# Kernel optimization log

Measured on AMD Instinct MI355X. Metric: run time of the kernel, lower is better.

## Reference

```python
import jax, jax.numpy as jnp
import numpy as np
from jax import lax

VOCAB, EMBED, HIDDEN = 32000, 512, 1024
BATCH, SEQ = 64, 512


def setup_inputs() -> dict:
    key = jax.random.key(0)
    ks = jax.random.split(key, 10)
    H, E, V = HIDDEN, EMBED, VOCAB
    s = lambda *d: 1.0 / np.sqrt(d[0])
    return {
        "x": jax.random.randint(ks[0], (BATCH, SEQ), 0, V, dtype=jnp.int32),
        "embed_table": jax.random.normal(ks[1], (V, E), jnp.float32) * 0.02,
        "Wx0": jax.random.normal(ks[2], (E, 4 * H), jnp.float32) * s(E),
        "Wh0": jax.random.normal(ks[3], (H, 4 * H), jnp.float32) * s(H),
        "b0": jnp.zeros((4 * H,), jnp.float32),
        "Wx1": jax.random.normal(ks[4], (H, 4 * H), jnp.float32) * s(H),
        "Wh1": jax.random.normal(ks[5], (H, 4 * H), jnp.float32) * s(H),
        "b1": jnp.zeros((4 * H,), jnp.float32),
        "Wout": jax.random.normal(ks[6], (H, V), jnp.float32) * s(H),
        "bout": jnp.zeros((V,), jnp.float32),
    }


def _lstm_layer(inp, Wx, Wh, b):
    # inp: [B, S, D_in] -> hidden states [B, S, H]
    B = inp.shape[0]
    H = Wh.shape[0]
    # Precompute the input projection for all timesteps (one big GEMM).
    x4 = jnp.einsum("bsd,dg->bsg", inp, Wx) + b           # [B, S, 4H]
    x4 = jnp.swapaxes(x4, 0, 1)                              # [S, B, 4H]
    h0 = jnp.zeros((B, H), inp.dtype)
    c0 = jnp.zeros((B, H), inp.dtype)

    def step(carry, xt4):
        h, c = carry
        g = xt4 + h @ Wh                                     # [B, 4H]
        i, f, gg, o = jnp.split(g, 4, axis=-1)
        c = jax.nn.sigmoid(f) * c + jax.nn.sigmoid(i) * jnp.tanh(gg)
        h = jax.nn.sigmoid(o) * jnp.tanh(c)
        return (h, c), h

    _, hs = lax.scan(step, (h0, c0), x4)                     # hs: [S, B, H]
    return jnp.swapaxes(hs, 0, 1)                            # [B, S, H]


def reference(x, embed_table, Wx0, Wh0, b0, Wx1, Wh1, b1, Wout, bout):
    emb = embed_table[x]                                      # [B, S, E]
    h1 = _lstm_layer(emb, Wx0, Wh0, b0)                       # [B, S, H]
    h2 = _lstm_layer(h1, Wx1, Wh1, b1)                        # [B, S, H]
    logits = h2[:, -1, :] @ Wout + bout                       # [B, V] (last timestep)
    return jax.nn.softmax(logits, axis=-1)
```

## Files before the change

kernel.cpp:

```cpp
#include <hip/hip_runtime.h>


#define BB 64
#define SS 512
#define EE 512
#define HH 1024
#define GG 4096
#define VV 32000

using bf16x8 = __attribute__((ext_vector_type(8))) __bf16;
using f32x4  = __attribute__((ext_vector_type(4))) float;

__device__ __forceinline__ unsigned short f2bf(float f) {
    unsigned u = __float_as_uint(f);
    unsigned r = u + 0x7FFFu + ((u >> 16) & 1u);
    return (unsigned short)(r >> 16);
}
__device__ __forceinline__ float bf2f(unsigned short u) {
    return __uint_as_float(((unsigned)u) << 16);
}
__device__ __forceinline__ float sigm(float x) {
    return 1.0f / (1.0f + expf(-x));
}
__device__ __forceinline__ bf16x8 ld_frag_coh(const unsigned long long* p) {
    union { unsigned long long u[2]; bf16x8 v; } x;
    x.u[0] = __hip_atomic_load(p,     __ATOMIC_RELAXED, __HIP_MEMORY_SCOPE_AGENT);
    x.u[1] = __hip_atomic_load(p + 1, __ATOMIC_RELAXED, __HIP_MEMORY_SCOPE_AGENT);
    return x.v;
}
__device__ __forceinline__ void gate_poll(const unsigned int* p, unsigned tgt) {
    while (__hip_atomic_load(p, __ATOMIC_RELAXED, __HIP_MEMORY_SCOPE_AGENT) < tgt)
        __builtin_amdgcn_s_sleep(1);
    __builtin_amdgcn_sched_barrier(0);
}

__global__ void pack_b(const float* __restrict__ B, unsigned short* __restrict__ out,
                       int KT, int N) {
    int bid = blockIdx.x;
    int lane = threadIdx.x;
    int nt = bid / KT, kt = bid % KT;
    int k = kt * 32 + ((lane >> 4) << 3);
    int n = nt * 16 + (lane & 15);
    size_t base = ((size_t)bid * 64 + lane) * 8;
    #pragma unroll
    for (int j = 0; j < 8; ++j)
        out[base + j] = f2bf(B[(size_t)(k + j) * N + n]);
}

__global__ void pack_wh(const float* __restrict__ Wh, unsigned short* __restrict__ out) {
    int f = blockIdx.x;
    int lane = threadIdx.x;
    int kt = f & 31, nt = (f >> 5) & 1, g = f >> 6;
    int nloc = lane & 15;
    int q = nt * 2 + (nloc >> 3), cj = nloc & 7;
    int gcol = q * HH + 8 * g + cj;
    int k = kt * 32 + ((lane >> 4) << 3);
    size_t base = ((size_t)f * 64 + lane) * 8;
    #pragma unroll
    for (int j = 0; j < 8; ++j)
        out[base + j] = f2bf(Wh[(size_t)(k + j) * GG + gcol]);
}

__global__ void embed_pack(const int* __restrict__ x, const float* __restrict__ tab,
                           unsigned short* __restrict__ out) {
    int bid = blockIdx.x;
    int lane = threadIdx.x;
    int mt = bid >> 4, kt = bid & 15;
    int m = mt * 16 + (lane & 15);
    int idx = x[(m & 63) * SS + (m >> 6)];
    int kb = kt * 32 + ((lane >> 4) << 3);
    size_t base = ((size_t)bid * 64 + lane) * 8;
    const float* src = tab + (size_t)idx * EE + kb;
    #pragma unroll
    for (int j = 0; j < 8; ++j)
        out[base + j] = f2bf(src[j]);
}

template<int MODE>
__global__ __launch_bounds__(256) void gemm_bias(
    const unsigned short* __restrict__ Ap, const unsigned short* __restrict__ Bp,
    const float* __restrict__ bias, void* __restrict__ Cout, int N, int KT) {
    __shared__ unsigned short tile[64][72];
    const int tid = threadIdx.x, lane = tid & 63, w = tid >> 6;
    const int ntg = blockIdx.x * 4 + w;
    const int m0t = blockIdx.y * 4;
    const bf16x8* Av = reinterpret_cast<const bf16x8*>(Ap);
    const bf16x8* Bv = reinterpret_cast<const bf16x8*>(Bp);
    f32x4 acc[4] = {{0.f,0.f,0.f,0.f},{0.f,0.f,0.f,0.f},{0.f,0.f,0.f,0.f},{0.f,0.f,0.f,0.f}};
    for (int kt = 0; kt < KT; ++kt) {
        bf16x8 b = Bv[((size_t)ntg * KT + kt) * 64 + lane];
        #pragma unroll
        for (int mt = 0; mt < 4; ++mt) {
            bf16x8 a = Av[((size_t)(m0t + mt) * KT + kt) * 64 + lane];
            acc[mt] = __builtin_amdgcn_mfma_f32_16x16x32_bf16(a, b, acc[mt], 0, 0, 0);
        }
    }
    const int col = ntg * 16 + (lane & 15);
    const int rq = (lane >> 4) << 2;
    const float bb = bias[col];
    if (MODE == 0) {
        #pragma unroll
        for (int mt = 0; mt < 4; ++mt)
            #pragma unroll
            for (int i = 0; i < 4; ++i) {
                int row = (m0t + mt) * 16 + rq + i;
                ((float*)Cout)[(size_t)row * N + col] = acc[mt][i] + bb;
            }
    } else {
        const int cl = w * 16 + (lane & 15);
        #pragma unroll
        for (int mt = 0; mt < 4; ++mt)
            #pragma unroll
            for (int i = 0; i < 4; ++i)
                tile[cl][mt * 16 + rq + i] = f2bf(acc[mt][i] + bb);
        __syncthreads();
        const int c = tid >> 2, b0 = (tid & 3) << 4;
        unsigned short* dst = (unsigned short*)Cout +
            ((size_t)blockIdx.y * GG + (size_t)blockIdx.x * 64) * 64 + (size_t)tid * 16;
        const uint4* s4 = reinterpret_cast<const uint4*>(&tile[c][b0]);
        reinterpret_cast<uint4*>(dst)[0] = s4[0];
        reinterpret_cast<uint4*>(dst)[1] = s4[1];
    }
}

__global__ void zero_init(unsigned short* __restrict__ h0a,
                          unsigned short* __restrict__ h0b,
                          unsigned int* __restrict__ flags) {
    int i = blockIdx.x * 256 + threadIdx.x;
    for (int k = i; k < BB * HH; k += 64 * 256) { h0a[k] = 0; h0b[k] = 0; }
    for (int k = i; k < 9216; k += 64 * 256) flags[k] = 0;
}

__global__ __launch_bounds__(256, 2) void lstm_fused(
    const unsigned short* __restrict__ x4s,
    const unsigned short* __restrict__ wh0p, const unsigned short* __restrict__ wh1p,
    const unsigned short* __restrict__ wx1p,
    const float* __restrict__ b1,
    unsigned short* __restrict__ hb0, unsigned short* __restrict__ hb1,
    unsigned short* __restrict__ hb2, unsigned short* __restrict__ hb3,
    unsigned int* __restrict__ flags) {
    __shared__ float gx[2][32][36];
    __shared__ __align__(16) unsigned short hlds[32][8];
    __shared__ __align__(16) unsigned short Blds[64 * 64 * 8];
    const int tid = threadIdx.x, lane = tid & 63, w = tid >> 6;
    const int L = (blockIdx.x >= 256) ? 1 : 0;
    const int inner = blockIdx.x & 255;
    const int g = inner >> 1, hf = inner & 1;
    unsigned int* done   = flags + L * 4096 + hf * 2048;
    unsigned int* go_own = flags + 8192 + (L * 2 + hf) * 256;
    unsigned int* go_oth = flags + 8192 + ((1 - L) * 2 + hf) * 256;
    const int rep = (g & 15) * 16;

    {
        const uint4* src = reinterpret_cast<const uint4*>(L ? wh1p : wh0p) + (size_t)g * 4096;
        uint4* dst = reinterpret_cast<uint4*>(Blds);
        #pragma unroll
        for (int i = 0; i < 16; ++i)
            dst[i * 256 + tid] = src[i * 256 + tid];
    }
    __syncthreads();
    const bf16x8* Bl = reinterpret_cast<const bf16x8*>(Blds);
    const bf16x8* Wx = reinterpret_cast<const bf16x8*>(wx1p);

    const int msub = w & 1, kh = w >> 1;
    const int kh16 = kh * 16;
    const int nloc = lane & 15;
    const int cj = nloc & 7;
    const int q0 = nloc >> 3;
    const int gq0 = q0 * HH + 8 * g + cj;
    const int gq1 = (2 + q0) * HH + 8 * g + cj;
    const int rbase = msub * 16 + ((lane >> 4) << 2);
    const size_t afrag_base = ((size_t)(2 * hf + msub) * 32 + (size_t)kh * 16) * 64 + lane;
    const int row_l = tid >> 3, cj2 = tid & 7;
    float c = 0.f;

    if (L == 0) {
        ushort4 xv0 = {0, 0, 0, 0}, xv1 = {0, 0, 0, 0};
        if (kh == 0) {
            xv0 = *reinterpret_cast<const ushort4*>(x4s + ((size_t)gq0) * 64 + 32 * hf + rbase);
            xv1 = *reinterpret_cast<const ushort4*>(x4s + ((size_t)gq1) * 64 + 32 * hf + rbase);
        }
        #pragma unroll 1
        for (int t = 0; t < SS; ++t) {
            if (t > 0) {
                gate_poll(&go_own[rep], (unsigned)t);
                if (t >= 2) gate_poll(&go_oth[rep], (unsigned)(t - 1));
            }
            const unsigned long long* hv =
                reinterpret_cast<const unsigned long long*>((t & 1) ? hb1 : hb0);
            unsigned short* hout = (t & 1) ? hb0 : hb1;

            bf16x8 A[16];
            #pragma unroll
            for (int k = 0; k < 16; ++k)
                A[k] = ld_frag_coh(hv + (afrag_base + (size_t)k * 64) * 2);

            f32x4 acc0 = {0.f, 0.f, 0.f, 0.f}, acc1 = {0.f, 0.f, 0.f, 0.f};
            #pragma unroll
            for (int k = 0; k < 16; ++k) {
                acc0 = __builtin_amdgcn_mfma_f32_16x16x32_bf16(
                    A[k], Bl[(kh16 + k) * 64 + lane], acc0, 0, 0, 0);
                acc1 = __builtin_amdgcn_mfma_f32_16x16x32_bf16(
                    A[k], Bl[(32 + kh16 + k) * 64 + lane], acc1, 0, 0, 0);
            }
            if (kh == 0) {
                gx[0][nloc][rbase + 0] = acc0[0] + bf2f(xv0.x);
                gx[0][nloc][rbase + 1] = acc0[1] + bf2f(xv0.y);
                gx[0][nloc][rbase + 2] = acc0[2] + bf2f(xv0.z);
                gx[0][nloc][rbase + 3] = acc0[3] + bf2f(xv0.w);
                gx[0][16 + nloc][rbase + 0] = acc1[0] + bf2f(xv1.x);
                gx[0][16 + nloc][rbase + 1] = acc1[1] + bf2f(xv1.y);
                gx[0][16 + nloc][rbase + 2] = acc1[2] + bf2f(xv1.z);
                gx[0][16 + nloc][rbase + 3] = acc1[3] + bf2f(xv1.w);
            } else {
                gx[1][nloc][rbase + 0] = acc0[0];
                gx[1][nloc][rbase + 1] = acc0[1];
                gx[1][nloc][rbase + 2] = acc0[2];
                gx[1][nloc][rbase + 3] = acc0[3];
                gx[1][16 + nloc][rbase + 0] = acc1[0];
                gx[1][16 + nloc][rbase + 1] = acc1[1];
                gx[1][16 + nloc][rbase + 2] = acc1[2];
                gx[1][16 + nloc][rbase + 3] = acc1[3];
            }
            __syncthreads();

            float gi = gx[0][0 * 8 + cj2][row_l] + gx[1][0 * 8 + cj2][row_l];
            float gf = gx[0][1 * 8 + cj2][row_l] + gx[1][1 * 8 + cj2][row_l];
            float gg = gx[0][2 * 8 + cj2][row_l] + gx[1][2 * 8 + cj2][row_l];
            float go = gx[0][3 * 8 + cj2][row_l] + gx[1][3 * 8 + cj2][row_l];
            float cn = sigm(gf) * c + sigm(gi) * tanhf(gg);
            c = cn;
            hlds[row_l][cj2] = f2bf(sigm(go) * tanhf(cn));
            __syncthreads();

            if (tid < 32) {
                union { uint4 v; unsigned long long u[2]; } cv;
                cv.v = *reinterpret_cast<const uint4*>(&hlds[tid][0]);
                const int m = 32 * hf + tid;
                unsigned long long* dst = reinterpret_cast<unsigned long long*>(
                    hout + (((size_t)(m >> 4) * 32 + (g >> 2)) * 64 + (g & 3) * 16 + (m & 15)) * 8);
                __hip_atomic_store(dst,     cv.u[0], __ATOMIC_RELAXED, __HIP_MEMORY_SCOPE_AGENT);
                __hip_atomic_store(dst + 1, cv.u[1], __ATOMIC_RELAXED, __HIP_MEMORY_SCOPE_AGENT);
            }
            if (w == 0)
                asm volatile("s_waitcnt vmcnt(0)" ::: "memory");
            if (tid == 0)
                __hip_atomic_store(&done[g * 16], (unsigned)(t + 1),
                                   __ATOMIC_RELAXED, __HIP_MEMORY_SCOPE_AGENT);
            if (kh == 0 && t + 1 < SS) {
                xv0 = *reinterpret_cast<const ushort4*>(
                    x4s + ((size_t)(t + 1) * GG + gq0) * 64 + 32 * hf + rbase);
                xv1 = *reinterpret_cast<const ushort4*>(
                    x4s + ((size_t)(t + 1) * GG + gq1) * 64 + 32 * hf + rbase);
            }
            if (g == 0 && tid < 64) {
                const unsigned tgt = (unsigned)(t + 1);
                unsigned v0 = 0, v1 = 0;
                while (1) {
                    if (v0 < tgt)
                        v0 = __hip_atomic_load(&done[tid * 16], __ATOMIC_RELAXED,
                                               __HIP_MEMORY_SCOPE_AGENT);
                    if (v1 < tgt)
                        v1 = __hip_atomic_load(&done[(tid + 64) * 16], __ATOMIC_RELAXED,
                                               __HIP_MEMORY_SCOPE_AGENT);
                    if (__all((v0 >= tgt) && (v1 >= tgt))) break;
                    __builtin_amdgcn_s_sleep(1);
                }
                if (tid < 16)
                    __hip_atomic_store(&go_own[tid * 16], tgt, __ATOMIC_RELAXED,
                                       __HIP_MEMORY_SCOPE_AGENT);
            }
        }
    } else {
        const float bb0 = b1[gq0], bb1 = b1[gq1];
        #pragma unroll 1
        for (int t = 0; t < SS; ++t) {
            gate_poll(&go_oth[rep], (unsigned)(t + 1));
            const unsigned long long* hv1 =
                reinterpret_cast<const unsigned long long*>((t & 1) ? hb0 : hb1);
            bf16x8 A1[16];
            #pragma unroll
            for (int k = 0; k < 16; ++k)
                A1[k] = ld_frag_coh(hv1 + (afrag_base + (size_t)k * 64) * 2);

            if (t > 0)
                gate_poll(&go_own[rep], (unsigned)t);
            const unsigned long long* hv2 =
                reinterpret_cast<const unsigned long long*>((t & 1) ? hb3 : hb2);
            unsigned short* hout2 = (t & 1) ? hb2 : hb3;
            bf16x8 A2[16];
            #pragma unroll
            for (int k = 0; k < 16; ++k)
                A2[k] = ld_frag_coh(hv2 + (afrag_base + (size_t)k * 64) * 2);

            f32x4 acc0 = {0.f, 0.f, 0.f, 0.f}, acc1 = {0.f, 0.f, 0.f, 0.f};
            {
                bf16x8 BXa[8], BXb[8];
                #pragma unroll
                for (int j = 0; j < 8; ++j) {
                    BXa[j] = Wx[((size_t)(g * 64 + kh16 + j)) * 64 + lane];
                    BXb[j] = Wx[((size_t)(g * 64 + 32 + kh16 + j)) * 64 + lane];
                }
                #pragma unroll
                for (int j = 0; j < 8; ++j) {
                    acc0 = __builtin_amdgcn_mfma_f32_16x16x32_bf16(A1[j], BXa[j], acc0, 0, 0, 0);
                    acc1 = __builtin_amdgcn_mfma_f32_16x16x32_bf16(A1[j], BXb[j], acc1, 0, 0, 0);
                }
                #pragma unroll
                for (int j = 0; j < 8; ++j) {
                    BXa[j] = Wx[((size_t)(g * 64 + kh16 + 8 + j)) * 64 + lane];
                    BXb[j] = Wx[((size_t)(g * 64 + 32 + kh16 + 8 + j)) * 64 + lane];
                }
                #pragma unroll
                for (int j = 0; j < 8; ++j) {
                    acc0 = __builtin_amdgcn_mfma_f32_16x16x32_bf16(A1[8 + j], BXa[j], acc0, 0, 0, 0);
                    acc1 = __builtin_amdgcn_mfma_f32_16x16x32_bf16(A1[8 + j], BXb[j], acc1, 0, 0, 0);
                }
            }
            #pragma unroll
            for (int k = 0; k < 16; ++k) {
                acc0 = __builtin_amdgcn_mfma_f32_16x16x32_bf16(
                    A2[k], Bl[(kh16 + k) * 64 + lane], acc0, 0, 0, 0);
                acc1 = __builtin_amdgcn_mfma_f32_16x16x32_bf16(
                    A2[k], Bl[(32 + kh16 + k) * 64 + lane], acc1, 0, 0, 0);
            }

            if (kh == 0) {
                gx[0][nloc][rbase + 0] = acc0[0] + bb0;
                gx[0][nloc][rbase + 1] = acc0[1] + bb0;
                gx[0][nloc][rbase + 2] = acc0[2] + bb0;
                gx[0][nloc][rbase + 3] = acc0[3] + bb0;
                gx[0][16 + nloc][rbase + 0] = acc1[0] + bb1;
                gx[0][16 + nloc][rbase + 1] = acc1[1] + bb1;
                gx[0][16 + nloc][rbase + 2] = acc1[2] + bb1;
                gx[0][16 + nloc][rbase + 3] = acc1[3] + bb1;
            } else {
                gx[1][nloc][rbase + 0] = acc0[0];
                gx[1][nloc][rbase + 1] = acc0[1];
                gx[1][nloc][rbase + 2] = acc0[2];
                gx[1][nloc][rbase + 3] = acc0[3];
                gx[1][16 + nloc][rbase + 0] = acc1[0];
                gx[1][16 + nloc][rbase + 1] = acc1[1];
                gx[1][16 + nloc][rbase + 2] = acc1[2];
                gx[1][16 + nloc][rbase + 3] = acc1[3];
            }
            __syncthreads();

            float gi = gx[0][0 * 8 + cj2][row_l] + gx[1][0 * 8 + cj2][row_l];
            float gf = gx[0][1 * 8 + cj2][row_l] + gx[1][1 * 8 + cj2][row_l];
            float gg = gx[0][2 * 8 + cj2][row_l] + gx[1][2 * 8 + cj2][row_l];
            float go = gx[0][3 * 8 + cj2][row_l] + gx[1][3 * 8 + cj2][row_l];
            float cn = sigm(gf) * c + sigm(gi) * tanhf(gg);
            c = cn;
            hlds[row_l][cj2] = f2bf(sigm(go) * tanhf(cn));
            __syncthreads();

            if (tid < 32) {
                union { uint4 v; unsigned long long u[2]; } cv;
                cv.v = *reinterpret_cast<const uint4*>(&hlds[tid][0]);
                const int m = 32 * hf + tid;
                unsigned long long* dst = reinterpret_cast<unsigned long long*>(
                    hout2 + (((size_t)(m >> 4) * 32 + (g >> 2)) * 64 + (g & 3) * 16 + (m & 15)) * 8);
                __hip_atomic_store(dst,     cv.u[0], __ATOMIC_RELAXED, __HIP_MEMORY_SCOPE_AGENT);
                __hip_atomic_store(dst + 1, cv.u[1], __ATOMIC_RELAXED, __HIP_MEMORY_SCOPE_AGENT);
            }
            if (w == 0)
                asm volatile("s_waitcnt vmcnt(0)" ::: "memory");
            if (tid == 0)
                __hip_atomic_store(&done[g * 16], (unsigned)(t + 1),
                                   __ATOMIC_RELAXED, __HIP_MEMORY_SCOPE_AGENT);
            if (g == 0 && tid < 64) {
                const unsigned tgt = (unsigned)(t + 1);
                unsigned v0 = 0, v1 = 0;
                while (1) {
                    if (v0 < tgt)
                        v0 = __hip_atomic_load(&done[tid * 16], __ATOMIC_RELAXED,
                                               __HIP_MEMORY_SCOPE_AGENT);
                    if (v1 < tgt)
                        v1 = __hip_atomic_load(&done[(tid + 64) * 16], __ATOMIC_RELAXED,
                                               __HIP_MEMORY_SCOPE_AGENT);
                    if (__all((v0 >= tgt) && (v1 >= tgt))) break;
                    __builtin_amdgcn_s_sleep(1);
                }
                if (tid < 16)
                    __hip_atomic_store(&go_own[tid * 16], tgt, __ATOMIC_RELAXED,
                                       __HIP_MEMORY_SCOPE_AGENT);
            }
        }
    }
}

__global__ __launch_bounds__(256) void softmax_rows(const float* __restrict__ logits,
                                                    float* __restrict__ out) {
    __shared__ float red[256];
    int rr = blockIdx.x, tid = threadIdx.x;
    const float* L = logits + (size_t)rr * VV;
    float m = -1e30f;
    for (int i = tid; i < VV; i += 256) m = fmaxf(m, L[i]);
    red[tid] = m; __syncthreads();
    for (int s = 128; s > 0; s >>= 1) { if (tid < s) red[tid] = fmaxf(red[tid], red[tid + s]); __syncthreads(); }
    m = red[0]; __syncthreads();
    float sum = 0.f;
    for (int i = tid; i < VV; i += 256) sum += expf(L[i] - m);
    red[tid] = sum; __syncthreads();
    for (int s = 128; s > 0; s >>= 1) { if (tid < s) red[tid] += red[tid + s]; __syncthreads(); }
    float inv = 1.f / red[0];
    for (int i = tid; i < VV; i += 256) out[(size_t)rr * VV + i] = expf(L[i] - m) * inv;
}

extern "C" void kernel_launch(void* const* d_in, const int* in_sizes, int n_in,
                              void* d_out, int out_size, void* d_ws, size_t ws_size,
                              hipStream_t stream) {
    const int*   x    = (const int*)  d_in[0];
    const float* tab  = (const float*)d_in[1];
    const float* Wx0  = (const float*)d_in[2];
    const float* Wh0  = (const float*)d_in[3];
    const float* b0   = (const float*)d_in[4];
    const float* Wx1  = (const float*)d_in[5];
    const float* Wh1  = (const float*)d_in[6];
    const float* b1   = (const float*)d_in[7];
    const float* Wout = (const float*)d_in[8];
    const float* bout = (const float*)d_in[9];
    float* out = (float*)d_out;

    unsigned short* ws    = (unsigned short*)d_ws;
    unsigned short* embA  = ws;
    unsigned short* wx0p  = embA  + 16777216;
    unsigned short* wh0p  = wx0p  + 2097152;
    unsigned short* wx1p  = wh0p  + 4194304;
    unsigned short* wh1p  = wx1p  + 4194304;
    unsigned short* woutp = wh1p  + 4194304;
    unsigned short* x4s   = woutp + 32768000;
    unsigned short* h1A   = x4s   + 134217728;
    unsigned short* hb0   = h1A   + 33554432;
    unsigned short* hb1   = hb0   + 65536;
    unsigned short* hb2   = hb1   + 65536;
    unsigned short* hb3   = hb2   + 65536;
    float* logits = (float*)(hb3 + 65536);
    unsigned int* flags = (unsigned int*)(logits + 2048000);

    pack_b <<<256 * 16, 64, 0, stream>>>(Wx0, wx0p, 16, GG);
    pack_wh<<<8192, 64, 0, stream>>>(Wh0, wh0p);
    pack_wh<<<8192, 64, 0, stream>>>(Wx1, wx1p);
    pack_wh<<<8192, 64, 0, stream>>>(Wh1, wh1p);
    pack_b <<<2000 * 32, 64, 0, stream>>>(Wout, woutp, 32, VV);

    zero_init<<<64, 256, 0, stream>>>(hb0, hb2, flags);

    embed_pack<<<32768, 64, 0, stream>>>(x, tab, embA);
    gemm_bias<1><<<dim3(GG / 64, 32768 / 64), 256, 0, stream>>>(embA, wx0p, b0, x4s, GG, EE / 32);

    {
        const unsigned short* a0 = x4s;
        const unsigned short* a1 = wh0p; const unsigned short* a2 = wh1p;
        const unsigned short* a3 = wx1p; const float* a4 = b1;
        unsigned short *a5 = hb0, *a6 = hb1, *a7 = hb2, *a8 = hb3;
        unsigned int* a9 = flags;
        void* args[] = {&a0, &a1, &a2, &a3, &a4, &a5, &a6, &a7, &a8, &a9};
        hipLaunchCooperativeKernel((const void*)lstm_fused, dim3(512), dim3(256),
                                   args, 0, stream);
    }

    gemm_bias<0><<<dim3(VV / 64, 1), 256, 0, stream>>>(hb2, woutp, bout, logits, VV, HH / 32);
    softmax_rows<<<64, 256, 0, stream>>>(logits, out);
}
```

Measured before the change: 3.885 ms.

## Run both LSTM layers in the same block with skewed wavefront schedule

```diff
diff --git a/kernel.cpp b/kernel.cpp
--- a/kernel.cpp
+++ b/kernel.cpp
@@ -131,7 +131,7 @@
     for (int k = i; k < 9216; k += 64 * 256) flags[k] = 0;
 }
 
-__global__ __launch_bounds__(256, 2) void lstm_fused(
+__global__ __launch_bounds__(256, 1) void lstm_fused(
     const unsigned short* __restrict__ x4s,
     const unsigned short* __restrict__ wh0p, const unsigned short* __restrict__ wh1p,
     const unsigned short* __restrict__ wx1p,
@@ -141,26 +141,29 @@
     unsigned int* __restrict__ flags) {
     __shared__ float gx[2][32][36];
     __shared__ __align__(16) unsigned short hlds[32][8];
-    __shared__ __align__(16) unsigned short Blds[64 * 64 * 8];
+    __shared__ __align__(16) unsigned short Blds0[64 * 64 * 8];
+    __shared__ __align__(16) unsigned short Blds1[64 * 64 * 8];
     const int tid = threadIdx.x, lane = tid & 63, w = tid >> 6;
-    const int L = (blockIdx.x >= 256) ? 1 : 0;
-    const int inner = blockIdx.x & 255;
-    const int g = inner >> 1, hf = inner & 1;
-    unsigned int* done   = flags + L * 4096 + hf * 2048;
-    unsigned int* go_own = flags + 8192 + (L * 2 + hf) * 256;
-    unsigned int* go_oth = flags + 8192 + ((1 - L) * 2 + hf) * 256;
+    const int g = blockIdx.x >> 1, hf = blockIdx.x & 1;
+    unsigned int* done = flags + hf * 2048;
+    unsigned int* goL  = flags + 8192 + hf * 256;
     const int rep = (g & 15) * 16;
 
     {
-        const uint4* src = reinterpret_cast<const uint4*>(L ? wh1p : wh0p) + (size_t)g * 4096;
-        uint4* dst = reinterpret_cast<uint4*>(Blds);
+        const uint4* s0 = reinterpret_cast<const uint4*>(wh0p) + (size_t)g * 4096;
+        const uint4* s1 = reinterpret_cast<const uint4*>(wh1p) + (size_t)g * 4096;
+        uint4* d0 = reinterpret_cast<uint4*>(Blds0);
+        uint4* d1 = reinterpret_cast<uint4*>(Blds1);
         #pragma unroll
-        for (int i = 0; i < 16; ++i)
-            dst[i * 256 + tid] = src[i * 256 + tid];
+        for (int i = 0; i < 16; ++i) {
+            d0[i * 256 + tid] = s0[i * 256 + tid];
+            d1[i * 256 + tid] = s1[i * 256 + tid];
+        }
     }
     __syncthreads();
-    const bf16x8* Bl = reinterpret_cast<const bf16x8*>(Blds);
-    const bf16x8* Wx = reinterpret_cast<const bf16x8*>(wx1p);
+    const bf16x8* Bl0 = reinterpret_cast<const bf16x8*>(Blds0);
+    const bf16x8* Bl1 = reinterpret_cast<const bf16x8*>(Blds1);
+    const bf16x8* Wx  = reinterpret_cast<const bf16x8*>(wx1p);
 
     const int msub = w & 1, kh = w >> 1;
     const int kh16 = kh * 16;
@@ -172,128 +175,48 @@
     const int rbase = msub * 16 + ((lane >> 4) << 2);
     const size_t afrag_base = ((size_t)(2 * hf + msub) * 32 + (size_t)kh * 16) * 64 + lane;
     const int row_l = tid >> 3, cj2 = tid & 7;
-    float c = 0.f;
-
-    if (L == 0) {
-        ushort4 xv0 = {0, 0, 0, 0}, xv1 = {0, 0, 0, 0};
-        if (kh == 0) {
-            xv0 = *reinterpret_cast<const ushort4*>(x4s + ((size_t)gq0) * 64 + 32 * hf + rbase);
-            xv1 = *reinterpret_cast<const ushort4*>(x4s + ((size_t)gq1) * 64 + 32 * hf + rbase);
-        }
-        #pragma unroll 1
-        for (int t = 0; t < SS; ++t) {
-            if (t > 0) {
-                gate_poll(&go_own[rep], (unsigned)t);
-                if (t >= 2) gate_poll(&go_oth[rep], (unsigned)(t - 1));
-            }
-            const unsigned long long* hv =
-                reinterpret_cast<const unsigned long long*>((t & 1) ? hb1 : hb0);
-            unsigned short* hout = (t & 1) ? hb0 : hb1;
-
-            bf16x8 A[16];
-            #pragma unroll
-            for (int k = 0; k < 16; ++k)
-                A[k] = ld_frag_coh(hv + (afrag_base + (size_t)k * 64) * 2);
-
-            f32x4 acc0 = {0.f, 0.f, 0.f, 0.f}, acc1 = {0.f, 0.f, 0.f, 0.f};
-            #pragma unroll
-            for (int k = 0; k < 16; ++k) {
-                acc0 = __builtin_amdgcn_mfma_f32_16x16x32_bf16(
-                    A[k], Bl[(kh16 + k) * 64 + lane], acc0, 0, 0, 0);
-                acc1 = __builtin_amdgcn_mfma_f32_16x16x32_bf16(
-                    A[k], Bl[(32 + kh16 + k) * 64 + lane], acc1, 0, 0, 0);
-            }
-            if (kh == 0) {
-                gx[0][nloc][rbase + 0] = acc0[0] + bf2f(xv0.x);
-                gx[0][nloc][rbase + 1] = acc0[1] + bf2f(xv0.y);
-                gx[0][nloc][rbase + 2] = acc0[2] + bf2f(xv0.z);
-                gx[0][nloc][rbase + 3] = acc0[3] + bf2f(xv0.w);
-                gx[0][16 + nloc][rbase + 0] = acc1[0] + bf2f(xv1.x);
-                gx[0][16 + nloc][rbase + 1] = acc1[1] + bf2f(xv1.y);
-                gx[0][16 + nloc][rbase + 2] = acc1[2] + bf2f(xv1.z);
-                gx[0][16 + nloc][rbase + 3] = acc1[3] + bf2f(xv1.w);
-            } else {
-                gx[1][nloc][rbase + 0] = acc0[0];
-                gx[1][nloc][rbase + 1] = acc0[1];
-                gx[1][nloc][rbase + 2] = acc0[2];
-                gx[1][nloc][rbase + 3] = acc0[3];
-                gx[1][16 + nloc][rbase + 0] = acc1[0];
-                gx[1][16 + nloc][rbase + 1] = acc1[1];
-                gx[1][16 + nloc][rbase + 2] = acc1[2];
-                gx[1][16 + nloc][rbase + 3] = acc1[3];
-            }
-            __syncthreads();
-
-            float gi = gx[0][0 * 8 + cj2][row_l] + gx[1][0 * 8 + cj2][row_l];
-            float gf = gx[0][1 * 8 + cj2][row_l] + gx[1][1 * 8 + cj2][row_l];
-            float gg = gx[0][2 * 8 + cj2][row_l] + gx[1][2 * 8 + cj2][row_l];
-            float go = gx[0][3 * 8 + cj2][row_l] + gx[1][3 * 8 + cj2][row_l];
-            float cn = sigm(gf) * c + sigm(gi) * tanhf(gg);
-            c = cn;
-            hlds[row_l][cj2] = f2bf(sigm(go) * tanhf(cn));
-            __syncthreads();
-
-            if (tid < 32) {
-                union { uint4 v; unsigned long long u[2]; } cv;
-                cv.v = *reinterpret_cast<const uint4*>(&hlds[tid][0]);
-                const int m = 32 * hf + tid;
-                unsigned long long* dst = reinterpret_cast<unsigned long long*>(
-                    hout + (((size_t)(m >> 4) * 32 + (g >> 2)) * 64 + (g & 3) * 16 + (m & 15)) * 8);
-                __hip_atomic_store(dst,     cv.u[0], __ATOMIC_RELAXED, __HIP_MEMORY_SCOPE_AGENT);
-                __hip_atomic_store(dst + 1, cv.u[1], __ATOMIC_RELAXED, __HIP_MEMORY_SCOPE_AGENT);
-            }
-            if (w == 0)
-                asm volatile("s_waitcnt vmcnt(0)" ::: "memory");
-            if (tid == 0)
-                __hip_atomic_store(&done[g * 16], (unsigned)(t + 1),
-                                   __ATOMIC_RELAXED, __HIP_MEMORY_SCOPE_AGENT);
-            if (kh == 0 && t + 1 < SS) {
-                xv0 = *reinterpret_cast<const ushort4*>(
-                    x4s + ((size_t)(t + 1) * GG + gq0) * 64 + 32 * hf + rbase);
-                xv1 = *reinterpret_cast<const ushort4*>(
-                    x4s + ((size_t)(t + 1) * GG + gq1) * 64 + 32 * hf + rbase);
-            }
-            if (g == 0 && tid < 64) {
-                const unsigned tgt = (unsigned)(t + 1);
-                unsigned v0 = 0, v1 = 0;
-                while (1) {
-                    if (v0 < tgt)
-                        v0 = __hip_atomic_load(&done[tid * 16], __ATOMIC_RELAXED,
-                                               __HIP_MEMORY_SCOPE_AGENT);
-                    if (v1 < tgt)
-                        v1 = __hip_atomic_load(&done[(tid + 64) * 16], __ATOMIC_RELAXED,
-                                               __HIP_MEMORY_SCOPE_AGENT);
-                    if (__all((v0 >= tgt) && (v1 >= tgt))) break;
-                    __builtin_amdgcn_s_sleep(1);
-                }
-                if (tid < 16)
-                    __hip_atomic_store(&go_own[tid * 16], tgt, __ATOMIC_RELAXED,
-                                       __HIP_MEMORY_SCOPE_AGENT);
-            }
-        }
-    } else {
-        const float bb0 = b1[gq0], bb1 = b1[gq1];
-        #pragma unroll 1
-        for (int t = 0; t < SS; ++t) {
-            gate_poll(&go_oth[rep], (unsigned)(t + 1));
-            const unsigned long long* hv1 =
-                reinterpret_cast<const unsigned long long*>((t & 1) ? hb0 : hb1);
-            bf16x8 A1[16];
-            #pragma unroll
-            for (int k = 0; k < 16; ++k)
-                A1[k] = ld_frag_coh(hv1 + (afrag_base + (size_t)k * 64) * 2);
-
-            if (t > 0)
-                gate_poll(&go_own[rep], (unsigned)t);
+    float c0 = 0.f, c1 = 0.f;
+    const float bb0 = b1[gq0], bb1 = b1[gq1];
+
+    ushort4 xv0 = {0, 0, 0, 0}, xv1 = {0, 0, 0, 0};
+    if (kh == 0) {
+        xv0 = *reinterpret_cast<const ushort4*>(x4s + ((size_t)gq0) * 64 + 32 * hf + rbase);
+        xv1 = *reinterpret_cast<const ushort4*>(x4s + ((size_t)gq1) * 64 + 32 * hf + rbase);
+    }
+
+    #pragma unroll 1
+    for (int t = 0; t <= SS; ++t) {
+        if (t > 0)
+            gate_poll(&goL[rep], (unsigned)t);
+
+        const unsigned long long* hv1 =
+            reinterpret_cast<const unsigned long long*>((t & 1) ? hb1 : hb0);
+        bf16x8 A[16];
+        #pragma unroll
+        for (int k = 0; k < 16; ++k)
+            A[k] = ld_frag_coh(hv1 + (afrag_base + (size_t)k * 64) * 2);
+
+        bf16x8 A2[16];
+        if (t >= 1) {
             const unsigned long long* hv2 =
-                reinterpret_cast<const unsigned long long*>((t & 1) ? hb3 : hb2);
-            unsigned short* hout2 = (t & 1) ? hb2 : hb3;
-            bf16x8 A2[16];
+                reinterpret_cast<const unsigned long long*>((t & 1) ? hb2 : hb3);
             #pragma unroll
             for (int k = 0; k < 16; ++k)
                 A2[k] = ld_frag_coh(hv2 + (afrag_base + (size_t)k * 64) * 2);
-
-            f32x4 acc0 = {0.f, 0.f, 0.f, 0.f}, acc1 = {0.f, 0.f, 0.f, 0.f};
+        }
+
+        f32x4 a00 = {0.f,0.f,0.f,0.f}, a01 = {0.f,0.f,0.f,0.f};
+        f32x4 a10 = {0.f,0.f,0.f,0.f}, a11 = {0.f,0.f,0.f,0.f};
+        if (t < SS) {
+            #pragma unroll
+            for (int k = 0; k < 16; ++k) {
+                a00 = __builtin_amdgcn_mfma_f32_16x16x32_bf16(
+                    A[k], Bl0[(kh16 + k) * 64 + lane], a00, 0, 0, 0);
+                a01 = __builtin_amdgcn_mfma_f32_16x16x32_bf16(
+                    A[k], Bl0[(32 + kh16 + k) * 64 + lane], a01, 0, 0, 0);
+            }
+        }
+        if (t >= 1) {
             {
                 bf16x8 BXa[8], BXb[8];
                 #pragma unroll
@@ -303,8 +226,8 @@
                 }
                 #pragma unroll
                 for (int j = 0; j < 8; ++j) {
-                    acc0 = __builtin_amdgcn_mfma_f32_16x16x32_bf16(A1[j], BXa[j], acc0, 0, 0, 0);
-                    acc1 = __builtin_amdgcn_mfma_f32_16x16x32_bf16(A1[j], BXb[j], acc1, 0, 0, 0);
+                    a10 = __builtin_amdgcn_mfma_f32_16x16x32_bf16(A[j], BXa[j], a10, 0, 0, 0);
+                    a11 = __builtin_amdgcn_mfma_f32_16x16x32_bf16(A[j], BXb[j], a11, 0, 0, 0);
                 }
                 #pragma unroll
                 for (int j = 0; j < 8; ++j) {
@@ -313,78 +236,129 @@
                 }
                 #pragma unroll
                 for (int j = 0; j < 8; ++j) {
-                    acc0 = __builtin_amdgcn_mfma_f32_16x16x32_bf16(A1[8 + j], BXa[j], acc0, 0, 0, 0);
-                    acc1 = __builtin_amdgcn_mfma_f32_16x16x32_bf16(A1[8 + j], BXb[j], acc1, 0, 0, 0);
+                    a10 = __builtin_amdgcn_mfma_f32_16x16x32_bf16(A[8 + j], BXa[j], a10, 0, 0, 0);
+                    a11 = __builtin_amdgcn_mfma_f32_16x16x32_bf16(A[8 + j], BXb[j], a11, 0, 0, 0);
                 }
             }
             #pragma unroll
             for (int k = 0; k < 16; ++k) {
-                acc0 = __builtin_amdgcn_mfma_f32_16x16x32_bf16(
-                    A2[k], Bl[(kh16 + k) * 64 + lane], acc0, 0, 0, 0);
-                acc1 = __builtin_amdgcn_mfma_f32_16x16x32_bf16(
-                    A2[k], Bl[(32 + kh16 + k) * 64 + lane], acc1, 0, 0, 0);
-            }
-
+                a10 = __builtin_amdgcn_mfma_f32_16x16x32_bf16(
+                    A2[k], Bl1[(kh16 + k) * 64 + lane], a10, 0, 0, 0);
+                a11 = __builtin_amdgcn_mfma_f32_16x16x32_bf16(
+                    A2[k], Bl1[(32 + kh16 + k) * 64 + lane], a11, 0, 0, 0);
+            }
+        }
+
+        if (t < SS) {
             if (kh == 0) {
-                gx[0][nloc][rbase + 0] = acc0[0] + bb0;
-                gx[0][nloc][rbase + 1] = acc0[1] + bb0;
-                gx[0][nloc][rbase + 2] = acc0[2] + bb0;
-                gx[0][nloc][rbase + 3] = acc0[3] + bb0;
-                gx[0][16 + nloc][rbase + 0] = acc1[0] + bb1;
-                gx[0][16 + nloc][rbase + 1] = acc1[1] + bb1;
-                gx[0][16 + nloc][rbase + 2] = acc1[2] + bb1;
-                gx[0][16 + nloc][rbase + 3] = acc1[3] + bb1;
+                gx[0][nloc][rbase + 0] = a00[0] + bf2f(xv0.x);
+                gx[0][nloc][rbase + 1] = a00[1] + bf2f(xv0.y);
+                gx[0][nloc][rbase + 2] = a00[2] + bf2f(xv0.z);
+                gx[0][nloc][rbase + 3] = a00[3] + bf2f(xv0.w);
+                gx[0][16 + nloc][rbase + 0] = a01[0] + bf2f(xv1.x);
+                gx[0][16 + nloc][rbase + 1] = a01[1] + bf2f(xv1.y);
+                gx[0][16 + nloc][rbase + 2] = a01[2] + bf2f(xv1.z);
+                gx[0][16 + nloc][rbase + 3] = a01[3] + bf2f(xv1.w);
             } else {
-                gx[1][nloc][rbase + 0] = acc0[0];
-                gx[1][nloc][rbase + 1] = acc0[1];
-                gx[1][nloc][rbase + 2] = acc0[2];
-                gx[1][nloc][rbase + 3] = acc0[3];
-                gx[1][16 + nloc][rbase + 0] = acc1[0];
-                gx[1][16 + nloc][rbase + 1] = acc1[1];
-                gx[1][16 + nloc][rbase + 2] = acc1[2];
-                gx[1][16 + nloc][rbase + 3] = acc1[3];
+                gx[1][nloc][rbase + 0] = a00[0];
+                gx[1][nloc][rbase + 1] = a00[1];
+                gx[1][nloc][rbase + 2] = a00[2];
+                gx[1][nloc][rbase + 3] = a00[3];
+                gx[1][16 + nloc][rbase + 0] = a01[0];
+                gx[1][16 + nloc][rbase + 1] = a01[1];
+                gx[1][16 + nloc][rbase + 2] = a01[2];
+                gx[1][16 + nloc][rbase + 3] = a01[3];
             }
             __syncthreads();
-
             float gi = gx[0][0 * 8 + cj2][row_l] + gx[1][0 * 8 + cj2][row_l];
             float gf = gx[0][1 * 8 + cj2][row_l] + gx[1][1 * 8 + cj2][row_l];
             float gg = gx[0][2 * 8 + cj2][row_l] + gx[1][2 * 8 + cj2][row_l];
             float go = gx[0][3 * 8 + cj2][row_l] + gx[1][3 * 8 + cj2][row_l];
-            float cn = sigm(gf) * c + sigm(gi) * tanhf(gg);
-            c = cn;
+            float cn = sigm(gf) * c0 + sigm(gi) * tanhf(gg);
+            c0 = cn;
             hlds[row_l][cj2] = f2bf(sigm(go) * tanhf(cn));
             __syncthreads();
-
             if (tid < 32) {
                 union { uint4 v; unsigned long long u[2]; } cv;
                 cv.v = *reinterpret_cast<const uint4*>(&hlds[tid][0]);
                 const int m = 32 * hf + tid;
+                unsigned short* hout1 = (t & 1) ? hb0 : hb1;
+                unsigned long long* dst = reinterpret_cast<unsigned long long*>(
+                    hout1 + (((size_t)(m >> 4) * 32 + (g >> 2)) * 64 + (g & 3) * 16 + (m & 15)) * 8);
+                __hip_atomic_store(dst,     cv.u[0], __ATOMIC_RELAXED, __HIP_MEMORY_SCOPE_AGENT);
+                __hip_atomic_store(dst + 1, cv.u[1], __ATOMIC_RELAXED, __HIP_MEMORY_SCOPE_AGENT);
+            }
+        }
+
+        if (t >= 1) {
+            if (kh == 0) {
+                gx[0][nloc][rbase + 0] = a10[0] + bb0;
+                gx[0][nloc][rbase + 1] = a10[1] + bb0;
+                gx[0][nloc][rbase + 2] = a10[2] + bb0;
+                gx[0][nloc][rbase + 3] = a10[3] + bb0;
+                gx[0][16 + nloc][rbase + 0] = a11[0] + bb1;
+                gx[0][16 + nloc][rbase + 1] = a11[1] + bb1;
+                gx[0][16 + nloc][rbase + 2] = a11[2] + bb1;
+                gx[0][16 + nloc][rbase + 3] = a11[3] + bb1;
+            } else {
+                gx[1][nloc][rbase + 0] = a10[0];
+                gx[1][nloc][rbase + 1] = a10[1];
+                gx[1][nloc][rbase + 2] = a10[2];
+                gx[1][nloc][rbase + 3] = a10[3];
+                gx[1][16 + nloc][rbase + 0] = a11[0];
+                gx[1][16 + nloc][rbase + 1] = a11[1];
+                gx[1][16 + nloc][rbase + 2] = a11[2];
+                gx[1][16 + nloc][rbase + 3] = a11[3];
+            }
+            __syncthreads();
+            float gi = gx[0][0 * 8 + cj2][row_l] + gx[1][0 * 8 + cj2][row_l];
+            float gf = gx[0][1 * 8 + cj2][row_l] + gx[1][1 * 8 + cj2][row_l];
+            float gg = gx[0][2 * 8 + cj2][row_l] + gx[1][2 * 8 + cj2][row_l];
+            float go = gx[0][3 * 8 + cj2][row_l] + gx[1][3 * 8 + cj2][row_l];
+            float cn = sigm(gf) * c1 + sigm(gi) * tanhf(gg);
+            c1 = cn;
+            hlds[row_l][cj2] = f2bf(sigm(go) * tanhf(cn));
+            __syncthreads();
+            if (tid < 32) {
+                union { uint4 v; unsigned long long u[2]; } cv;
+                cv.v = *reinterpret_cast<const uint4*>(&hlds[tid][0]);
+                const int m = 32 * hf + tid;
+                unsigned short* hout2 = (t & 1) ? hb3 : hb2;
                 unsigned long long* dst = reinterpret_cast<unsigned long long*>(
                     hout2 + (((size_t)(m >> 4) * 32 + (g >> 2)) * 64 + (g & 3) * 16 + (m & 15)) * 8);
                 __hip_atomic_store(dst,     cv.u[0], __ATOMIC_RELAXED, __HIP_MEMORY_SCOPE_AGENT);
                 __hip_atomic_store(dst + 1, cv.u[1], __ATOMIC_RELAXED, __HIP_MEMORY_SCOPE_AGENT);
             }
+        }
+
+        if (t < SS) {
             if (w == 0)
                 asm volatile("s_waitcnt vmcnt(0)" ::: "memory");
             if (tid == 0)
                 __hip_atomic_store(&done[g * 16], (unsigned)(t + 1),
                                    __ATOMIC_RELAXED, __HIP_MEMORY_SCOPE_AGENT);
-            if (g == 0 && tid < 64) {
+            if (g == 0 && w == 3) {
                 const unsigned tgt = (unsigned)(t + 1);
                 unsigned v0 = 0, v1 = 0;
                 while (1) {
                     if (v0 < tgt)
-                        v0 = __hip_atomic_load(&done[tid * 16], __ATOMIC_RELAXED,
+                        v0 = __hip_atomic_load(&done[lane * 16], __ATOMIC_RELAXED,
                                                __HIP_MEMORY_SCOPE_AGENT);
                     if (v1 < tgt)
-                        v1 = __hip_atomic_load(&done[(tid + 64) * 16], __ATOMIC_RELAXED,
+                        v1 = __hip_atomic_load(&done[(lane + 64) * 16], __ATOMIC_RELAXED,
                                                __HIP_MEMORY_SCOPE_AGENT);
                     if (__all((v0 >= tgt) && (v1 >= tgt))) break;
                     __builtin_amdgcn_s_sleep(1);
                 }
-                if (tid < 16)
-                    __hip_atomic_store(&go_own[tid * 16], tgt, __ATOMIC_RELAXED,
+                if (lane < 16)
+                    __hip_atomic_store(&goL[lane * 16], tgt, __ATOMIC_RELAXED,
                                        __HIP_MEMORY_SCOPE_AGENT);
+            }
+            if (kh == 0 && t + 1 < SS) {
+                xv0 = *reinterpret_cast<const ushort4*>(
+                    x4s + ((size_t)(t + 1) * GG + gq0) * 64 + 32 * hf + rbase);
+                xv1 = *reinterpret_cast<const ushort4*>(
+                    x4s + ((size_t)(t + 1) * GG + gq1) * 64 + 32 * hf + rbase);
             }
         }
     }
@@ -431,8 +405,7 @@
     unsigned short* wh1p  = wx1p  + 4194304;
     unsigned short* woutp = wh1p  + 4194304;
     unsigned short* x4s   = woutp + 32768000;
-    unsigned short* h1A   = x4s   + 134217728;
-    unsigned short* hb0   = h1A   + 33554432;
+    unsigned short* hb0   = x4s   + 134217728;
     unsigned short* hb1   = hb0   + 65536;
     unsigned short* hb2   = hb1   + 65536;
     unsigned short* hb3   = hb2   + 65536;
@@ -457,7 +430,7 @@
         unsigned short *a5 = hb0, *a6 = hb1, *a7 = hb2, *a8 = hb3;
         unsigned int* a9 = flags;
         void* args[] = {&a0, &a1, &a2, &a3, &a4, &a5, &a6, &a7, &a8, &a9};
-        hipLaunchCooperativeKernel((const void*)lstm_fused, dim3(512), dim3(256),
+        hipLaunchCooperativeKernel((const void*)lstm_fused, dim3(256), dim3(256),
                                    args, 0, stream);
     }
 
```

New measurement: 5.947 ms. 53.1% more time.
